# Performance work log

Measured on AMD Instinct MI355X. Metric: run time of the kernel, lower is better.

Reference implementation:

```python
import jax, jax.numpy as jnp
import numpy as np

Q_HEADS, KV_HEADS, HEAD_DIM, WINDOW = 16, 4, 128, 512
HIDDEN = 2048
ROPE_BASE = 10000.0


def _rope_tables(T, head_dim, dtype):
    half = head_dim // 2
    inv_freq = 1.0 / (ROPE_BASE ** (jnp.arange(half, dtype=jnp.float32) / half))
    t = jnp.arange(T, dtype=jnp.float32)
    freqs = jnp.outer(t, inv_freq)  # [T, half]
    return jnp.cos(freqs).astype(dtype), jnp.sin(freqs).astype(dtype)


def _apply_rope(x, cos, sin):
    # x: [B, T, H, D]; cos/sin: [T, D//2] -> broadcast [1, T, 1, D//2]
    c = cos[None, :, None, :]
    s = sin[None, :, None, :]
    x1, x2 = jnp.split(x, 2, axis=-1)
    return jnp.concatenate([x1 * c - x2 * s, x1 * s + x2 * c], axis=-1)


def setup_inputs() -> dict:
    key = jax.random.key(0)
    ks = jax.random.split(key, 5)
    B, T = 1, 4096
    x = jax.random.normal(ks[0], (B, T, HIDDEN), dtype=jnp.float32)
    sc = 0.02
    wq = jax.random.normal(ks[1], (Q_HEADS * HEAD_DIM, HIDDEN), dtype=jnp.float32) * sc
    wk = jax.random.normal(ks[2], (KV_HEADS * HEAD_DIM, HIDDEN), dtype=jnp.float32) * sc
    wv = jax.random.normal(ks[3], (KV_HEADS * HEAD_DIM, HIDDEN), dtype=jnp.float32) * sc
    wo = jax.random.normal(ks[4], (HIDDEN, Q_HEADS * HEAD_DIM), dtype=jnp.float32) * sc
    return {"x": x, "wq": wq, "wk": wk, "wv": wv, "wo": wo}


def reference(x, wq, wk, wv, wo):
    B, T, _ = x.shape
    reps = Q_HEADS // KV_HEADS
    scale = 1.0 / np.sqrt(HEAD_DIM)

    q = jnp.einsum('bth,oh->bto', x, wq).reshape(B, T, Q_HEADS, HEAD_DIM)
    k = jnp.einsum('bth,oh->bto', x, wk).reshape(B, T, KV_HEADS, HEAD_DIM)
    v = jnp.einsum('bth,oh->bto', x, wv).reshape(B, T, KV_HEADS, HEAD_DIM)

    cos, sin = _rope_tables(T, HEAD_DIM, x.dtype)
    q = _apply_rope(q, cos, sin)
    k = _apply_rope(k, cos, sin)

    # GQA without materializing repeated K/V: group q as [B,T,KVH,reps,D]
    qg = q.reshape(B, T, KV_HEADS, reps, HEAD_DIM)
    scores = jnp.einsum('btgrd,bsgd->bgrts', qg, k) * scale  # [B,KVH,reps,T,T]

    idx = jnp.arange(T)
    # allowed: causal (s <= t) AND within window (t - s <= WINDOW)
    allowed = (idx[None, :] <= idx[:, None]) & (idx[:, None] - idx[None, :] <= WINDOW)
    scores = jnp.where(allowed[None, None, None], scores, jnp.finfo(scores.dtype).min)
    probs = jax.nn.softmax(scores, axis=-1)

    out = jnp.einsum('bgrts,bsgd->btgrd', probs, v)  # [B,T,KVH,reps,D]
    out = out.reshape(B, T, Q_HEADS * HEAD_DIM)
    return jnp.einsum('bto,ho->bth', out, wo)
```

## Files before the change

### kernel.cpp

```cpp
#include <hip/hip_runtime.h>

typedef __attribute__((ext_vector_type(8))) short short8;
typedef __attribute__((ext_vector_type(4))) float f32x4;
typedef __attribute__((ext_vector_type(4))) unsigned short u16x4;

__device__ __forceinline__ unsigned short f2b(float f) {
  unsigned int u = __float_as_uint(f);
  u += 0x7fffu + ((u >> 16) & 1u);
  return (unsigned short)(u >> 16);
}
__device__ __forceinline__ void glds16(const void* g, void* l) {
  __builtin_amdgcn_global_load_lds(
      (const __attribute__((address_space(1))) unsigned int*)g,
      (__attribute__((address_space(3))) unsigned int*)l, 16, 0, 0);
}

__global__ __launch_bounds__(256) void cast_all(const float* __restrict__ x,
                                                const float* __restrict__ wq,
                                                const float* __restrict__ wk,
                                                const float* __restrict__ wv,
                                                const float* __restrict__ wo,
                                                unsigned short* __restrict__ dst) {
  const int i = blockIdx.x * 256 + threadIdx.x;
  const float* s;
  int off;
  if (i < 2097152)      { s = x;  off = i; }
  else if (i < 3145728) { s = wq; off = i - 2097152; }
  else if (i < 3407872) { s = wk; off = i - 3145728; }
  else if (i < 3670016) { s = wv; off = i - 3407872; }
  else                  { s = wo; off = i - 3670016; }
  f32x4 v = ((const f32x4*)s)[off];
  u16x4 o;
  o[0] = f2b(v[0]); o[1] = f2b(v[1]); o[2] = f2b(v[2]); o[3] = f2b(v[3]);
  ((u16x4*)dst)[i] = o;
}

#define BARF()                            \
  asm volatile("" ::: "memory");          \
  __builtin_amdgcn_s_barrier();           \
  asm volatile("" ::: "memory");

__global__ __launch_bounds__(512, 4) void gemm_t128(
    const unsigned short* __restrict__ A, const unsigned short* __restrict__ B,
    const int mode,
    unsigned short* __restrict__ qb, unsigned short* __restrict__ kb,
    unsigned short* __restrict__ vtg, float* __restrict__ Cout) {
  extern __shared__ char smem[];
  const int tid = threadIdx.x;
  const int w = tid >> 6, lane = tid & 63;
  const int quad = lane >> 4, l15 = lane & 15;
  const int wm = w >> 2, wn = w & 3;
  const int m0 = blockIdx.x * 128;
  const int y  = blockIdx.y;
  const int n0 = y * 128;

  int cb[2];
  cb[0] = mode ? wn : wn * 2;
  cb[1] = mode ? wn + 4 : wn * 2 + 1;

  const int fragOff = l15 * 64 + ((quad * 16) ^ ((l15 & 8) << 2));
  const int sr = lane >> 2;
  const int sc = ((lane & 3) * 8) ^ ((lane & 32) ? 16 : 0);
  const unsigned short* const Abase = A + (size_t)(m0 + (w >> 1) * 16 + sr) * 2048 + (w & 1) * 32 + sc;
  const unsigned short* const Bbase = B + (size_t)(n0 + (w >> 1) * 16 + sr) * 2048 + (w & 1) * 32 + sc;

#define T_STAGE_A(tt)                                                                    \
  {                                                                                      \
    const int t_ = ((tt) < 32) ? (tt) : 31;                                              \
    char* const d_ = smem + (t_ & 1) * 32768 + w * 1024;                                 \
    glds16(Abase + (size_t)t_ * 64, d_);                                                 \
    glds16(Abase + (64 * 2048) + (size_t)t_ * 64, d_ + 8192);                            \
  }
#define T_STAGE_B(tt)                                                                    \
  {                                                                                      \
    const int t_ = ((tt) < 32) ? (tt) : 31;                                              \
    char* const d_ = smem + (t_ & 1) * 32768 + 16384 + w * 1024;                         \
    glds16(Bbase + (size_t)t_ * 64, d_);                                                 \
    glds16(Bbase + (64 * 2048) + (size_t)t_ * 64, d_ + 8192);                            \
  }
#define T_RD_AHI(c)                                                                      \
  _Pragma("unroll") for (int mi = 2; mi < 4; ++mi)                                       \
  _Pragma("unroll") for (int kk = 0; kk < 2; ++kk)                                       \
      af[mi][kk] = *(const short8*)(smem + (c) * 32768 + ((wm * 4 + mi) * 2 + kk) * 1024 + fragOff);
#define T_RD_ALO(c)                                                                      \
  _Pragma("unroll") for (int mi = 0; mi < 2; ++mi)                                       \
  _Pragma("unroll") for (int kk = 0; kk < 2; ++kk)                                       \
      af[mi][kk] = *(const short8*)(smem + (c) * 32768 + ((wm * 4 + mi) * 2 + kk) * 1024 + fragOff);
#define T_RD_B(c)                                                                        \
  _Pragma("unroll") for (int ni = 0; ni < 2; ++ni)                                       \
  _Pragma("unroll") for (int kk = 0; kk < 2; ++kk)                                       \
      bf[ni][kk] = *(const short8*)(smem + (c) * 32768 + 16384 + (cb[ni] * 2 + kk) * 1024 + fragOff);

  f32x4 acc[4][2];
  const f32x4 fz = {0.f, 0.f, 0.f, 0.f};
#pragma unroll
  for (int i = 0; i < 4; ++i) { acc[i][0] = fz; acc[i][1] = fz; }

  short8 af[4][2], bf[2][2];

#define T_MFMA(MI0)                                                              \
  _Pragma("unroll") for (int kk = 0; kk < 2; ++kk)                               \
  _Pragma("unroll") for (int mi = 0; mi < 2; ++mi)                               \
  _Pragma("unroll") for (int ni = 0; ni < 2; ++ni)                               \
      acc[(MI0) + mi][ni] = __builtin_amdgcn_mfma_f32_16x16x32_bf16(             \
          af[(MI0) + mi][kk], bf[ni][kk], acc[(MI0) + mi][ni], 0, 0, 0);

  T_STAGE_A(0) T_STAGE_B(0) T_STAGE_A(1)
  asm volatile("s_waitcnt vmcnt(2)" ::: "memory");
  BARF()

#define T_TILE(c, tt)                                                                \
   T_RD_AHI(c)                                                               \
  asm volatile("" ::: "memory");                                                     \
  T_RD_ALO(c) T_RD_B(c)                                                              \
  T_STAGE_B((tt) + 1)                                                                \
  BARF()                                                                             \
  __builtin_amdgcn_s_setprio(1); T_MFMA(0) __builtin_amdgcn_s_setprio(0);            \
  BARF()                                                                             \
   T_STAGE_A((tt) + 2)                                                       \
  BARF()                                                                             \
  __builtin_amdgcn_s_setprio(1); T_MFMA(2) __builtin_amdgcn_s_setprio(0);            \
  asm volatile("s_waitcnt vmcnt(2)" ::: "memory");                                   \
  BARF()

#pragma unroll 1
  for (int T = 0; T < 32; T += 2) {
    T_TILE(0, T)
    T_TILE(1, T + 1)
  }
  asm volatile("s_waitcnt vmcnt(0)" ::: "memory");
#undef T_TILE
#undef T_MFMA
#undef T_RD_AHI
#undef T_RD_ALO
#undef T_RD_B
#undef T_STAGE_A
#undef T_STAGE_B

  const int tb0 = m0 + wm * 64;
  if (mode == 0) {
#pragma unroll
    for (int mi = 0; mi < 4; ++mi) {
      const int row = tb0 + mi * 16 + quad * 4;
#pragma unroll
      for (int ni = 0; ni < 2; ++ni) {
        const int col = n0 + cb[ni] * 16 + l15;
#pragma unroll
        for (int r = 0; r < 4; ++r)
          Cout[(size_t)(row + r) * 2048 + col] = acc[mi][ni][r];
      }
    }
    return;
  }
  if (y >= 20) {
    const int g = y - 20;
#pragma unroll
    for (int mi = 0; mi < 4; ++mi) {
      const int tb = tb0 + mi * 16 + quad * 4;
#pragma unroll
      for (int ni = 0; ni < 2; ++ni) {
        const int d = cb[ni] * 16 + l15;
        u16x4 o;
#pragma unroll
        for (int r = 0; r < 4; ++r) o[r] = f2b(acc[mi][ni][r]);
        *(u16x4*)(vtg + (size_t)(g * 128 + d) * 4096 + tb) = o;
      }
    }
  } else {
    unsigned short* dst;
    int stride, hoff;
    if (y < 16) { dst = qb; stride = 2048; hoff = y * 128; }
    else        { dst = kb; stride = 512;  hoff = (y - 16) * 128; }
    const float c2 = 0.20762050593045889f;
    const float inv2pi = 0.15915494309189535f;
    const int i = wn * 16 + l15;
    const float inv_rev = exp2f(-(float)i * c2) * inv2pi;
#pragma unroll
    for (int mi = 0; mi < 4; ++mi) {
#pragma unroll
      for (int r = 0; r < 4; ++r) {
        const int t = tb0 + mi * 16 + quad * 4 + r;
        float rev = (float)t * inv_rev;
        rev -= floorf(rev);
        const float sn = __builtin_amdgcn_sinf(rev);
        const float cs = __builtin_amdgcn_cosf(rev);
        const float x1 = acc[mi][0][r], x2 = acc[mi][1][r];
        unsigned short* p = dst + (size_t)t * stride + hoff + i;
        p[0]  = f2b(x1 * cs - x2 * sn);
        p[64] = f2b(x1 * sn + x2 * cs);
      }
    }
  }
}

__global__ __launch_bounds__(512, 2) void gemm128(const unsigned short* __restrict__ A,
                                                  const unsigned short* __restrict__ B,
                                                  float* __restrict__ Cout) {
  extern __shared__ char smem[];
  const int tid = threadIdx.x;
  const int w = tid >> 6, lane = tid & 63;
  const int quad = lane >> 4, l15 = lane & 15;
  const int wm = w >> 2, wn = w & 3;
  const int m0 = blockIdx.x * 128, n0 = blockIdx.y * 256;

  const int fragOff = l15 * 64 + ((quad * 16) ^ ((l15 & 8) << 2));
  char* const aWave = smem;
  char* const bWave = smem + 16384 + (wn >> 1) * 16384;

  const int sr = lane >> 2;
  const int sc = ((lane & 3) * 8) ^ ((lane & 32) ? 16 : 0);
  const unsigned short* const Abase = A + (size_t)(m0 + (w >> 1) * 16 + sr) * 2048 + (w & 1) * 32 + sc;
  const unsigned short* const Bbase = B + (size_t)(n0 + (w >> 1) * 16 + sr) * 2048 + (w & 1) * 32 + sc;

#define G_STAGE_A(tt)                                                                    \
  {                                                                                      \
    const int t_ = ((tt) < 32) ? (tt) : 31;                                              \
    char* const d_ = smem + (t_ & 1) * 49152 + w * 1024;                                 \
    glds16(Abase + (size_t)t_ * 64, d_);                                                 \
    glds16(Abase + (64 * 2048) + (size_t)t_ * 64, d_ + 8192);                            \
  }
#define G_STAGE_B(h, tt)                                                                 \
  {                                                                                      \
    const int t_ = ((tt) < 32) ? (tt) : 31;                                              \
    char* const d_ = smem + (t_ & 1) * 49152 + 16384 + (h) * 16384 + w * 1024;           \
    glds16(Bbase + (size_t)(h) * (128 * 2048) + (size_t)t_ * 64, d_);                    \
    glds16(Bbase + (size_t)(h) * (128 * 2048) + (64 * 2048) + (size_t)t_ * 64, d_ + 8192); \
  }
#define G_RD_A(c)                                                                        \
  _Pragma("unroll") for (int mi = 0; mi < 4; ++mi)                                       \
  _Pragma("unroll") for (int kk = 0; kk < 2; ++kk)                                       \
      af[mi][kk] = *(const short8*)(aWave + (c) * 49152 + ((wm * 4 + mi) * 2 + kk) * 1024 + fragOff);
#define G_RD_B(dst, c, NI0)                                                              \
  _Pragma("unroll") for (int ni = 0; ni < 2; ++ni)                                       \
  _Pragma("unroll") for (int kk = 0; kk < 2; ++kk)                                       \
      dst[ni][kk] = *(const short8*)(bWave + (c) * 49152 + (((wn & 1) * 4 + (NI0) + ni) * 2 + kk) * 1024 + fragOff);

  f32x4 acc[4][4];
  const f32x4 fz = {0.f, 0.f, 0.f, 0.f};
#pragma unroll
  for (int i = 0; i < 4; ++i)
#pragma unroll
    for (int j = 0; j < 4; ++j) acc[i][j] = fz;

  short8 af[4][2], blo[2][2], bhi[2][2];

#define G_MFMA(NOFF, BF)                                                         \
  _Pragma("unroll") for (int kk = 0; kk < 2; ++kk)                               \
  _Pragma("unroll") for (int mi = 0; mi < 4; ++mi)                               \
  _Pragma("unroll") for (int ni = 0; ni < 2; ++ni)                               \
      acc[mi][(NOFF) + ni] = __builtin_amdgcn_mfma_f32_16x16x32_bf16(            \
          af[mi][kk], BF[ni][kk], acc[mi][(NOFF) + ni], 0, 0, 0);

  G_STAGE_A(0) G_STAGE_B(0, 0) G_STAGE_B(1, 0) G_STAGE_A(1)
  asm volatile("s_waitcnt vmcnt(2)" ::: "memory");
  BARF()

#define G_TILE(c, tt)                                                                \
   G_RD_A(c) G_RD_B(blo, (c), 0)                                             \
  G_STAGE_B(0, (tt) + 1) G_STAGE_B(1, (tt) + 1)                                      \
  BARF()                                                                             \
  __builtin_amdgcn_s_setprio(1); G_MFMA(0, blo) __builtin_amdgcn_s_setprio(0);       \
  BARF()                                                                             \
   G_RD_B(bhi, (c), 2)                                                       \
  G_STAGE_A((tt) + 2)                                                                \
  BARF()                                                                             \
  __builtin_amdgcn_s_setprio(1); G_MFMA(2, bhi) __builtin_amdgcn_s_setprio(0);       \
  asm volatile("s_waitcnt vmcnt(2)" ::: "memory");                                   \
  BARF()

#pragma unroll 1
  for (int T = 0; T < 32; T += 2) {
    G_TILE(0, T)
    G_TILE(1, T + 1)
  }
  asm volatile("s_waitcnt vmcnt(0)" ::: "memory");
#undef G_TILE
#undef G_MFMA
#undef G_RD_A
#undef G_RD_B
#undef G_STAGE_A
#undef G_STAGE_B

  const int colBase = n0 + wn * 64;
#pragma unroll
  for (int mi = 0; mi < 4; ++mi) {
    const int row = m0 + wm * 64 + mi * 16 + quad * 4;
#pragma unroll
    for (int ni = 0; ni < 4; ++ni) {
      const int col = colBase + ni * 16 + l15;
#pragma unroll
      for (int r = 0; r < 4; ++r)
        Cout[(size_t)(row + r) * 2048 + col] = acc[mi][ni][r];
    }
  }
}

__global__ __launch_bounds__(512) void attn_fwd(const unsigned short* __restrict__ qp,
                                                const unsigned short* __restrict__ kp,
                                                const unsigned short* __restrict__ vtg,
                                                unsigned short* __restrict__ op) {
  __shared__ unsigned short Ks[2][4][1024];
  __shared__ unsigned short Vt[2][4096];
  const int tid = threadIdx.x;
  const int w = tid >> 6, lane = tid & 63;
  const int quad = lane >> 4, l15 = lane & 15;
  const int t0 = blockIdx.x * 64;
  const int g = blockIdx.y;
  const int h = g * 4 + (w & 3);
  const int t0w = t0 + (w >> 2) * 32;
  const f32x4 fzero = {0.f, 0.f, 0.f, 0.f};
  const float scale = 0.088388347648318447f;
  const float NEG_INF = -__builtin_inff();

  short8 qf[4][2];
#pragma unroll
  for (int qt = 0; qt < 2; qt++) {
    const unsigned short* qrow = qp + (size_t)(t0w + qt * 16 + l15) * 2048 + h * 128 + quad * 8;
#pragma unroll
    for (int kb = 0; kb < 4; kb++) qf[kb][qt] = *(const short8*)(qrow + kb * 32);
  }

  f32x4 oacc[8][2];
#pragma unroll
  for (int db = 0; db < 8; db++) { oacc[db][0] = fzero; oacc[db][1] = fzero; }
  float Mrow[2] = {-1.0e30f, -1.0e30f}, Lrow[2] = {0.f, 0.f};

  const int s_begin = (t0 >= 512) ? (t0 - 512) : 0;
  const int nch = ((t0 + 63 - s_begin) >> 5) + 1;

  const int r4 = lane >> 2, c4 = lane & 3;
#define ATTN_STAGE(s0_, b_)                                                              \
  {                                                                                      \
    const int s0v = (s0_);                                                               \
    if (w < 4) {                                                                         \
      _Pragma("unroll")                                                                  \
      for (int p = 0; p < 2; p++)                                                        \
        glds16(kp + (size_t)(s0v + p * 16 + r4) * 512 + g * 128 + w * 32 + c4 * 8,       \
               &Ks[b_][w][p * 512]);                                                     \
    } else {                                                                             \
      const int wv = w - 4;                                                              \
      _Pragma("unroll")                                                                  \
      for (int p = 0; p < 2; p++)                                                        \
        glds16(vtg + (size_t)(g * 128 + wv * 32 + p * 16 + r4) * 4096 + s0v + c4 * 8,    \
               &Vt[b_][wv * 1024 + p * 512]);                                            \
    }                                                                                    \
  }

  ATTN_STAGE(s_begin, 0);

  for (int c = 0; c < nch; ++c) {
    const int s0 = s_begin + c * 32;
    const int b = c & 1;
    __syncthreads();
    if (c + 1 < nch) ATTN_STAGE(s_begin + (c + 1) * 32, (c + 1) & 1);

    if (s0 + 31 >= t0w - 512 && s0 <= t0w + 31) {
      f32x4 sacc[2][2];
      sacc[0][0] = fzero; sacc[0][1] = fzero; sacc[1][0] = fzero; sacc[1][1] = fzero;
      const int permBase = ((l15 >> 2) << 3) + (l15 & 3);
#pragma unroll
      for (int kb = 0; kb < 4; kb++) {
        short8 af0 = *(const short8*)&Ks[b][kb][(permBase + 0) * 32 + quad * 8];
        short8 af1 = *(const short8*)&Ks[b][kb][(permBase + 4) * 32 + quad * 8];
        sacc[0][0] = __builtin_amdgcn_mfma_f32_16x16x32_bf16(af0, qf[kb][0], sacc[0][0], 0, 0, 0);
        sacc[0][1] = __builtin_amdgcn_mfma_f32_16x16x32_bf16(af0, qf[kb][1], sacc[0][1], 0, 0, 0);
        sacc[1][0] = __builtin_amdgcn_mfma_f32_16x16x32_bf16(af1, qf[kb][0], sacc[1][0], 0, 0, 0);
        sacc[1][1] = __builtin_amdgcn_mfma_f32_16x16x32_bf16(af1, qf[kb][1], sacc[1][1], 0, 0, 0);
      }

      short8 pb[2];
      float alpha[2];
#pragma unroll
      for (int qt = 0; qt < 2; qt++) {
        const int tq = t0w + qt * 16 + l15;
        float vals[8];
        float cmax = NEG_INF;
#pragma unroll
        for (int kt = 0; kt < 2; kt++)
#pragma unroll
          for (int r = 0; r < 4; r++) {
            const int s = s0 + quad * 8 + kt * 4 + r;
            const bool ok = (unsigned)(tq - s) <= 512u;
            const float v = ok ? sacc[kt][qt][r] * scale : NEG_INF;
            vals[kt * 4 + r] = v;
            cmax = fmaxf(cmax, v);
          }
        cmax = fmaxf(cmax, __shfl_xor(cmax, 16));
        cmax = fmaxf(cmax, __shfl_xor(cmax, 32));
        const float Mnew = fmaxf(Mrow[qt], cmax);
        alpha[qt] = __expf(Mrow[qt] - Mnew);
        Mrow[qt] = Mnew;
        float csum = 0.f;
#pragma unroll
        for (int j = 0; j < 8; j++) {
          const float p = __expf(vals[j] - Mnew);
          csum += p;
          pb[qt][j] = (short)f2b(p);
        }
        csum += __shfl_xor(csum, 16);
        csum += __shfl_xor(csum, 32);
        Lrow[qt] = Lrow[qt] * alpha[qt] + csum;
      }

#pragma unroll
      for (int db = 0; db < 8; db++) {
        short8 vf = *(const short8*)&Vt[b][(db * 16 + l15) * 32 + quad * 8];
#pragma unroll
        for (int qt = 0; qt < 2; qt++) {
          oacc[db][qt][0] *= alpha[qt]; oacc[db][qt][1] *= alpha[qt];
          oacc[db][qt][2] *= alpha[qt]; oacc[db][qt][3] *= alpha[qt];
          oacc[db][qt] = __builtin_amdgcn_mfma_f32_16x16x32_bf16(vf, pb[qt], oacc[db][qt], 0, 0, 0);
        }
      }
    }
  }
#undef ATTN_STAGE

#pragma unroll
  for (int qt = 0; qt < 2; qt++) {
    const float invL = 1.f / Lrow[qt];
    unsigned short* orow = op + (size_t)(t0w + qt * 16 + l15) * 2048 + h * 128;
#pragma unroll
    for (int db = 0; db < 8; db++) {
      u16x4 o;
#pragma unroll
      for (int r = 0; r < 4; r++) o[r] = f2b(oacc[db][qt][r] * invL);
      *(u16x4*)(orow + db * 16 + quad * 4) = o;
    }
  }
}

extern "C" void kernel_launch(void* const* d_in, const int* in_sizes, int n_in,
                              void* d_out, int out_size, void* d_ws, size_t ws_size,
                              hipStream_t stream) {
  const float* x  = (const float*)d_in[0];
  const float* wq = (const float*)d_in[1];
  const float* wk = (const float*)d_in[2];
  const float* wv = (const float*)d_in[3];
  const float* wo = (const float*)d_in[4];
  float* out = (float*)d_out;
  char* ws = (char*)d_ws;

  unsigned short* xb    = (unsigned short*)(ws + 0);
  unsigned short* wqkv  = (unsigned short*)(ws + 16777216);
  unsigned short* wob   = (unsigned short*)(ws + 29360128);
  unsigned short* qb    = (unsigned short*)(ws + 37748736);
  unsigned short* kbuf  = (unsigned short*)(ws + 54525952);
  unsigned short* vtg   = (unsigned short*)(ws + 58720256);
  unsigned short* attnb = xb;

  static bool attr_done = false;
  if (!attr_done) {
    hipFuncSetAttribute(reinterpret_cast<const void*>(gemm_t128),
                        hipFuncAttributeMaxDynamicSharedMemorySize, 65536);
    hipFuncSetAttribute(reinterpret_cast<const void*>(gemm128),
                        hipFuncAttributeMaxDynamicSharedMemorySize, 98304);
    attr_done = true;
  }

  cast_all<<<18432, 256, 0, stream>>>(x, wq, wk, wv, wo, (unsigned short*)ws);

  gemm_t128<<<dim3(32, 24), 512, 65536, stream>>>(xb, wqkv, 1, qb, kbuf, vtg, nullptr);

  attn_fwd<<<dim3(64, 4), 512, 0, stream>>>(qb, kbuf, vtg, attnb);

  gemm128<<<dim3(32, 8), 512, 98304, stream>>>(attnb, wob, out);
}
```

Measured before the change: 238.8 us.

## Halve attention block size and reuse gemm_t128 for output projection

The attention kernel now uses 256-thread blocks covering 32 query rows instead of 512 threads covering 64 rows. Each wave stages both K and V and processes every chunk without a per-wave skip test. This doubles the grid and removes the wasted chunks that one half of the old block had to skip. The separate gemm128 output projection kernel is deleted and replaced by the generic gemm_t128 in fp32-output mode with a smaller tile and a larger grid, trading the hand-tuned pipeline for better occupancy and simpler code.

```diff
diff --git a/kernel.cpp b/kernel.cpp
--- a/kernel.cpp
+++ b/kernel.cpp
@@ -193,109 +193,7 @@
   }
 }
 
-__global__ __launch_bounds__(512, 2) void gemm128(const unsigned short* __restrict__ A,
-                                                  const unsigned short* __restrict__ B,
-                                                  float* __restrict__ Cout) {
-  extern __shared__ char smem[];
-  const int tid = threadIdx.x;
-  const int w = tid >> 6, lane = tid & 63;
-  const int quad = lane >> 4, l15 = lane & 15;
-  const int wm = w >> 2, wn = w & 3;
-  const int m0 = blockIdx.x * 128, n0 = blockIdx.y * 256;
-
-  const int fragOff = l15 * 64 + ((quad * 16) ^ ((l15 & 8) << 2));
-  char* const aWave = smem;
-  char* const bWave = smem + 16384 + (wn >> 1) * 16384;
-
-  const int sr = lane >> 2;
-  const int sc = ((lane & 3) * 8) ^ ((lane & 32) ? 16 : 0);
-  const unsigned short* const Abase = A + (size_t)(m0 + (w >> 1) * 16 + sr) * 2048 + (w & 1) * 32 + sc;
-  const unsigned short* const Bbase = B + (size_t)(n0 + (w >> 1) * 16 + sr) * 2048 + (w & 1) * 32 + sc;
-
-#define G_STAGE_A(tt)                                                                    \
-  {                                                                                      \
-    const int t_ = ((tt) < 32) ? (tt) : 31;                                              \
-    char* const d_ = smem + (t_ & 1) * 49152 + w * 1024;                                 \
-    glds16(Abase + (size_t)t_ * 64, d_);                                                 \
-    glds16(Abase + (64 * 2048) + (size_t)t_ * 64, d_ + 8192);                            \
-  }
-#define G_STAGE_B(h, tt)                                                                 \
-  {                                                                                      \
-    const int t_ = ((tt) < 32) ? (tt) : 31;                                              \
-    char* const d_ = smem + (t_ & 1) * 49152 + 16384 + (h) * 16384 + w * 1024;           \
-    glds16(Bbase + (size_t)(h) * (128 * 2048) + (size_t)t_ * 64, d_);                    \
-    glds16(Bbase + (size_t)(h) * (128 * 2048) + (64 * 2048) + (size_t)t_ * 64, d_ + 8192); \
-  }
-#define G_RD_A(c)                                                                        \
-  _Pragma("unroll") for (int mi = 0; mi < 4; ++mi)                                       \
-  _Pragma("unroll") for (int kk = 0; kk < 2; ++kk)                                       \
-      af[mi][kk] = *(const short8*)(aWave + (c) * 49152 + ((wm * 4 + mi) * 2 + kk) * 1024 + fragOff);
-#define G_RD_B(dst, c, NI0)                                                              \
-  _Pragma("unroll") for (int ni = 0; ni < 2; ++ni)                                       \
-  _Pragma("unroll") for (int kk = 0; kk < 2; ++kk)                                       \
-      dst[ni][kk] = *(const short8*)(bWave + (c) * 49152 + (((wn & 1) * 4 + (NI0) + ni) * 2 + kk) * 1024 + fragOff);
-
-  f32x4 acc[4][4];
-  const f32x4 fz = {0.f, 0.f, 0.f, 0.f};
-#pragma unroll
-  for (int i = 0; i < 4; ++i)
-#pragma unroll
-    for (int j = 0; j < 4; ++j) acc[i][j] = fz;
-
-  short8 af[4][2], blo[2][2], bhi[2][2];
-
-#define G_MFMA(NOFF, BF)                                                         \
-  _Pragma("unroll") for (int kk = 0; kk < 2; ++kk)                               \
-  _Pragma("unroll") for (int mi = 0; mi < 4; ++mi)                               \
-  _Pragma("unroll") for (int ni = 0; ni < 2; ++ni)                               \
-      acc[mi][(NOFF) + ni] = __builtin_amdgcn_mfma_f32_16x16x32_bf16(            \
-          af[mi][kk], BF[ni][kk], acc[mi][(NOFF) + ni], 0, 0, 0);
-
-  G_STAGE_A(0) G_STAGE_B(0, 0) G_STAGE_B(1, 0) G_STAGE_A(1)
-  asm volatile("s_waitcnt vmcnt(2)" ::: "memory");
-  BARF()
-
-#define G_TILE(c, tt)                                                                \
-   G_RD_A(c) G_RD_B(blo, (c), 0)                                             \
-  G_STAGE_B(0, (tt) + 1) G_STAGE_B(1, (tt) + 1)                                      \
-  BARF()                                                                             \
-  __builtin_amdgcn_s_setprio(1); G_MFMA(0, blo) __builtin_amdgcn_s_setprio(0);       \
-  BARF()                                                                             \
-   G_RD_B(bhi, (c), 2)                                                       \
-  G_STAGE_A((tt) + 2)                                                                \
-  BARF()                                                                             \
-  __builtin_amdgcn_s_setprio(1); G_MFMA(2, bhi) __builtin_amdgcn_s_setprio(0);       \
-  asm volatile("s_waitcnt vmcnt(2)" ::: "memory");                                   \
-  BARF()
-
-#pragma unroll 1
-  for (int T = 0; T < 32; T += 2) {
-    G_TILE(0, T)
-    G_TILE(1, T + 1)
-  }
-  asm volatile("s_waitcnt vmcnt(0)" ::: "memory");
-#undef G_TILE
-#undef G_MFMA
-#undef G_RD_A
-#undef G_RD_B
-#undef G_STAGE_A
-#undef G_STAGE_B
-
-  const int colBase = n0 + wn * 64;
-#pragma unroll
-  for (int mi = 0; mi < 4; ++mi) {
-    const int row = m0 + wm * 64 + mi * 16 + quad * 4;
-#pragma unroll
-    for (int ni = 0; ni < 4; ++ni) {
-      const int col = colBase + ni * 16 + l15;
-#pragma unroll
-      for (int r = 0; r < 4; ++r)
-        Cout[(size_t)(row + r) * 2048 + col] = acc[mi][ni][r];
-    }
-  }
-}
-
-__global__ __launch_bounds__(512) void attn_fwd(const unsigned short* __restrict__ qp,
+__global__ __launch_bounds__(256) void attn_fwd(const unsigned short* __restrict__ qp,
                                                 const unsigned short* __restrict__ kp,
                                                 const unsigned short* __restrict__ vtg,
                                                 unsigned short* __restrict__ op) {
@@ -304,10 +202,9 @@
   const int tid = threadIdx.x;
   const int w = tid >> 6, lane = tid & 63;
   const int quad = lane >> 4, l15 = lane & 15;
-  const int t0 = blockIdx.x * 64;
+  const int t0 = blockIdx.x * 32;
   const int g = blockIdx.y;
-  const int h = g * 4 + (w & 3);
-  const int t0w = t0 + (w >> 2) * 32;
+  const int h = g * 4 + w;
   const f32x4 fzero = {0.f, 0.f, 0.f, 0.f};
   const float scale = 0.088388347648318447f;
   const float NEG_INF = -__builtin_inff();
@@ -315,7 +212,7 @@
   short8 qf[4][2];
 #pragma unroll
   for (int qt = 0; qt < 2; qt++) {
-    const unsigned short* qrow = qp + (size_t)(t0w + qt * 16 + l15) * 2048 + h * 128 + quad * 8;
+    const unsigned short* qrow = qp + (size_t)(t0 + qt * 16 + l15) * 2048 + h * 128 + quad * 8;
 #pragma unroll
     for (int kb = 0; kb < 4; kb++) qf[kb][qt] = *(const short8*)(qrow + kb * 32);
   }
@@ -326,24 +223,20 @@
   float Mrow[2] = {-1.0e30f, -1.0e30f}, Lrow[2] = {0.f, 0.f};
 
   const int s_begin = (t0 >= 512) ? (t0 - 512) : 0;
-  const int nch = ((t0 + 63 - s_begin) >> 5) + 1;
+  const int nch = ((t0 + 31 - s_begin) >> 5) + 1;
 
   const int r4 = lane >> 2, c4 = lane & 3;
 #define ATTN_STAGE(s0_, b_)                                                              \
   {                                                                                      \
     const int s0v = (s0_);                                                               \
-    if (w < 4) {                                                                         \
-      _Pragma("unroll")                                                                  \
-      for (int p = 0; p < 2; p++)                                                        \
-        glds16(kp + (size_t)(s0v + p * 16 + r4) * 512 + g * 128 + w * 32 + c4 * 8,       \
-               &Ks[b_][w][p * 512]);                                                     \
-    } else {                                                                             \
-      const int wv = w - 4;                                                              \
-      _Pragma("unroll")                                                                  \
-      for (int p = 0; p < 2; p++)                                                        \
-        glds16(vtg + (size_t)(g * 128 + wv * 32 + p * 16 + r4) * 4096 + s0v + c4 * 8,    \
-               &Vt[b_][wv * 1024 + p * 512]);                                            \
-    }                                                                                    \
+    _Pragma("unroll")                                                                    \
+    for (int p = 0; p < 2; p++)                                                          \
+      glds16(kp + (size_t)(s0v + p * 16 + r4) * 512 + g * 128 + w * 32 + c4 * 8,         \
+             &Ks[b_][w][p * 512]);                                                       \
+    _Pragma("unroll")                                                                    \
+    for (int p = 0; p < 2; p++)                                                          \
+      glds16(vtg + (size_t)(g * 128 + w * 32 + p * 16 + r4) * 4096 + s0v + c4 * 8,       \
+             &Vt[b_][w * 1024 + p * 512]);                                               \
   }
 
   ATTN_STAGE(s_begin, 0);
@@ -354,7 +247,7 @@
     __syncthreads();
     if (c + 1 < nch) ATTN_STAGE(s_begin + (c + 1) * 32, (c + 1) & 1);
 
-    if (s0 + 31 >= t0w - 512 && s0 <= t0w + 31) {
+    {
       f32x4 sacc[2][2];
       sacc[0][0] = fzero; sacc[0][1] = fzero; sacc[1][0] = fzero; sacc[1][1] = fzero;
       const int permBase = ((l15 >> 2) << 3) + (l15 & 3);
@@ -372,7 +265,7 @@
       float alpha[2];
 #pragma unroll
       for (int qt = 0; qt < 2; qt++) {
-        const int tq = t0w + qt * 16 + l15;
+        const int tq = t0 + qt * 16 + l15;
         float vals[8];
         float cmax = NEG_INF;
 #pragma unroll
@@ -419,7 +312,7 @@
 #pragma unroll
   for (int qt = 0; qt < 2; qt++) {
     const float invL = 1.f / Lrow[qt];
-    unsigned short* orow = op + (size_t)(t0w + qt * 16 + l15) * 2048 + h * 128;
+    unsigned short* orow = op + (size_t)(t0 + qt * 16 + l15) * 2048 + h * 128;
 #pragma unroll
     for (int db = 0; db < 8; db++) {
       u16x4 o;
@@ -453,8 +346,6 @@
   if (!attr_done) {
     hipFuncSetAttribute(reinterpret_cast<const void*>(gemm_t128),
                         hipFuncAttributeMaxDynamicSharedMemorySize, 65536);
-    hipFuncSetAttribute(reinterpret_cast<const void*>(gemm128),
-                        hipFuncAttributeMaxDynamicSharedMemorySize, 98304);
     attr_done = true;
   }
 
@@ -462,7 +353,8 @@
 
   gemm_t128<<<dim3(32, 24), 512, 65536, stream>>>(xb, wqkv, 1, qb, kbuf, vtg, nullptr);
 
-  attn_fwd<<<dim3(64, 4), 512, 0, stream>>>(qb, kbuf, vtg, attnb);
-
-  gemm128<<<dim3(32, 8), 512, 98304, stream>>>(attnb, wob, out);
-}
+  attn_fwd<<<dim3(128, 4), 256, 0, stream>>>(qb, kbuf, vtg, attnb);
+
+  gemm_t128<<<dim3(32, 16), 512, 65536, stream>>>(attnb, wob, 0,
+                                                  nullptr, nullptr, nullptr, out);
+}
```

New measurement: 255.3 us. 6.9% more time.
